# Kernel tuning notes

Measured on AMD Instinct MI355X. Metric: run time of the kernel, lower is better.

The kernel has to match this reference:

```python
import jax, jax.numpy as jnp
import numpy as np

N1, N2, D = 8192, 8192, 128

def setup_inputs() -> dict:
    key = jax.random.key(0)
    k1, k2 = jax.random.split(key)
    p1 = jax.random.normal(k1, (N1, D), dtype=jnp.float32)
    p2 = jax.random.normal(k2, (N2, D), dtype=jnp.float32)
    return {"p1": p1, "p2": p2}

def reference(p1, p2):
    # scores: [N1, N2]
    scores = jnp.matmul(p1, p2.T)
    # NOTE: original torch code MULTIPLIES by sqrt(N2) (not divide) — faithful.
    scale = jnp.asarray(scores.shape[-1], scores.dtype) ** 0.5
    weight = jax.nn.softmax(scores * scale, axis=-1)
    return jnp.matmul(weight, p2)  # [N1, D]
```

## Files before the change

kernel.cpp:

```cpp
#include <hip/hip_runtime.h>

#define NROWS 8192
#define DH 128
#define NTILES 256
#define NWAVES 4
#define BQ_WG 128
#define TILE_SHORTS 12288

typedef float f32x16 __attribute__((ext_vector_type(16)));
typedef float f32x4  __attribute__((ext_vector_type(4)));
typedef short s16x8  __attribute__((ext_vector_type(8)));

#define MFMA(a, b, c) __builtin_amdgcn_mfma_f32_32x32x16_bf16(a, b, c, 0, 0, 0)
#define EXP2F(x) __builtin_amdgcn_exp2f(x)

__device__ __forceinline__ short f2bf(float x) {
    unsigned u = __float_as_uint(x);
    unsigned r = (u + 0x7fffu + ((u >> 16) & 1u)) >> 16;
    return (short)r;
}
__device__ __forceinline__ float bf2f(short s) {
    return __uint_as_float(((unsigned)(unsigned short)s) << 16);
}

#define CSC 130.577849f

__device__ __forceinline__ void gload16(const short* g, short* l) {
    __builtin_amdgcn_global_load_lds(
        (const __attribute__((address_space(1))) unsigned*)g,
        (__attribute__((address_space(3))) unsigned*)l, 16, 0, 0);
}

__global__ __launch_bounds__(256) void prep(const float* __restrict__ KV,
                                            short* __restrict__ kws)
{
    const int t = blockIdx.x;
    const int tid = threadIdx.x;
    short* kh = kws + (size_t)t * TILE_SHORTS;
    short* kl = kh + 4096;
    short* vt = kh + 8192;

    {
        const int r  = tid >> 3;
        const int d0 = (tid & 7) << 4;
        const float* src = KV + ((size_t)(t * 32 + r)) * DH + d0;
        f32x4 a0 = *(const f32x4*)(src);
        f32x4 a1 = *(const f32x4*)(src + 4);
        f32x4 a2 = *(const f32x4*)(src + 8);
        f32x4 a3 = *(const f32x4*)(src + 12);
        s16x8 h0, h1, l0, l1;
        #pragma unroll
        for (int j = 0; j < 4; ++j) {
            { float x = a0[j]; short h = f2bf(x); h0[j]     = h; l0[j]     = f2bf(x - bf2f(h)); }
            { float x = a1[j]; short h = f2bf(x); h0[j + 4] = h; l0[j + 4] = f2bf(x - bf2f(h)); }
            { float x = a2[j]; short h = f2bf(x); h1[j]     = h; l1[j]     = f2bf(x - bf2f(h)); }
            { float x = a3[j]; short h = f2bf(x); h1[j + 4] = h; l1[j + 4] = f2bf(x - bf2f(h)); }
        }
        const int base = r * 128 + d0;
        const int swz  = (r & 7) << 3;
        *(s16x8*)&kh[(base    ) ^ swz] = h0;
        *(s16x8*)&kh[(base + 8) ^ swz] = h1;
        *(s16x8*)&kl[(base    ) ^ swz] = l0;
        *(s16x8*)&kl[(base + 8) ^ swz] = l1;
    }

    {
        const int pr = tid & 15;
        const int c8 = tid >> 4;
        const int r0 = pr * 2;
        const float* sa = KV + ((size_t)(t * 32 + r0)) * DH + c8 * 8;
        const float* sb = sa + DH;
        f32x4 a0 = *(const f32x4*)(sa);
        f32x4 a1 = *(const f32x4*)(sa + 4);
        f32x4 b0 = *(const f32x4*)(sb);
        f32x4 b1 = *(const f32x4*)(sb + 4);
        #pragma unroll
        for (int i = 0; i < 8; ++i) {
            int d = c8 * 8 + i;
            float xa = (i < 4) ? a0[i] : a1[i - 4];
            float xb = (i < 4) ? b0[i] : b1[i - 4];
            unsigned w = ((unsigned)(unsigned short)f2bf(xb) << 16) |
                         (unsigned short)f2bf(xa);
            int idx = (d * 32 + r0) ^ (((d >> 1) & 3) << 3);
            *(unsigned*)&vt[idx] = w;
        }
    }
}

__global__ __launch_bounds__(256, 2) void fa_partial(
    const float* __restrict__ Qm, const short* __restrict__ kws,
    float* __restrict__ Opart, float* __restrict__ mlbuf, int tiles_per_split)
{
    __shared__ __align__(16) short buf[2][TILE_SHORTS];
    __shared__ __align__(16) short pb[NWAVES][32 * 64];

    const int tid  = threadIdx.x;
    const int wid  = tid >> 6;
    const int lane = tid & 63;
    const int q32  = lane & 31;
    const int g    = lane >> 5;
    const int qb   = blockIdx.x;
    const int sp   = blockIdx.y;
    const int tile0 = sp * tiles_per_split;

    s16x8 qh[8], ql[8];
    {
        const float* qrow = Qm + ((size_t)(qb * BQ_WG + wid * 32 + q32)) * DH + g * 8;
        #pragma unroll
        for (int c = 0; c < 8; ++c) {
            const float* p = qrow + c * 16;
            f32x4 v0 = *(const f32x4*)(p);
            f32x4 v1 = *(const f32x4*)(p + 4);
            #pragma unroll
            for (int j = 0; j < 8; ++j) {
                float x = ((j < 4) ? v0[j] : v1[j - 4]) * CSC;
                short h = f2bf(x);
                qh[c][j] = h;
                ql[c][j] = f2bf(x - bf2f(h));
            }
        }
    }

    f32x16 oacc[4];
    #pragma unroll
    for (int b = 0; b < 4; ++b)
        #pragma unroll
        for (int i = 0; i < 16; ++i) oacc[b][i] = 0.0f;
    float mrun = -INFINITY;
    float lrun = 0.0f;

#define STAGE(bb, tt) do {                                              \
        const short* gs_ = kws + (size_t)(tt) * TILE_SHORTS + tid * 8;  \
        short* ld_ = &buf[bb][tid * 8];                                 \
        _Pragma("unroll")                                               \
        for (int ch_ = 0; ch_ < 6; ++ch_)                               \
            gload16(gs_ + ch_ * 2048, ld_ + ch_ * 2048);                \
    } while (0)

    int cur = 0;
    STAGE(0, tile0);

    for (int t = 0; t < tiles_per_split; ++t) {
        __syncthreads();
        if (t + 1 < tiles_per_split) STAGE(cur ^ 1, tile0 + t + 1);

        const short* kh = &buf[cur][0];
        const short* kl = &buf[cur][4096];
        const short* vt = &buf[cur][8192];

        f32x16 s;
        #pragma unroll
        for (int i = 0; i < 16; ++i) s[i] = 0.0f;
        #pragma unroll
        for (int c = 0; c < 8; ++c) {
            const int ia = (q32 * 128 + c * 16 + g * 8) ^ ((q32 & 7) << 3);
            s16x8 ah = *(const s16x8*)&kh[ia];
            s16x8 al = *(const s16x8*)&kl[ia];
            s = MFMA(ah, ql[c], s);
            s = MFMA(al, qh[c], s);
            s = MFMA(ah, qh[c], s);
        }

        float tmax = s[0];
        #pragma unroll
        for (int i = 1; i < 16; ++i) tmax = fmaxf(tmax, s[i]);
        tmax = fmaxf(tmax, __shfl_xor(tmax, 32));
        const float mnew  = fmaxf(mrun, tmax);
        const float alpha = EXP2F(mrun - mnew);
        float psum = 0.0f;
        #pragma unroll
        for (int i = 0; i < 16; ++i) { s[i] = EXP2F(s[i] - mnew); psum += s[i]; }
        psum += __shfl_xor(psum, 32);
        lrun = lrun * alpha + psum;
        if (__any(mnew > mrun)) {
            #pragma unroll
            for (int rI = 0; rI < 16; ++rI) {
                int qr = (rI & 3) + 8 * (rI >> 2) + 4 * g;
                float ar = __shfl(alpha, qr);
                #pragma unroll
                for (int b = 0; b < 4; ++b) oacc[b][rI] *= ar;
            }
        }
        mrun = mnew;

        {
            short* pw = pb[wid];
            #pragma unroll
            for (int pr2 = 0; pr2 < 8; ++pr2) {
                int rI = pr2 * 2;
                int k  = (rI & 3) + 8 * (rI >> 2) + 4 * g;
                unsigned w = ((unsigned)(unsigned short)f2bf(s[rI + 1]) << 16) |
                             (unsigned short)f2bf(s[rI]);
                int idx = (q32 * 64 + k) ^ ((q32 & 7) << 3);
                *(unsigned*)&pw[idx] = w;
            }
        }

        #pragma unroll
        for (int c2 = 0; c2 < 2; ++c2) {
            const int ip = (q32 * 64 + c2 * 16 + g * 8) ^ ((q32 & 7) << 3);
            s16x8 pa = *(const s16x8*)&pb[wid][ip];
            #pragma unroll
            for (int b = 0; b < 4; ++b) {
                int d  = b * 32 + q32;
                int iv = (d * 32 + c2 * 16 + g * 8) ^ (((d >> 1) & 3) << 3);
                s16x8 vv = *(const s16x8*)&vt[iv];
                oacc[b] = MFMA(pa, vv, oacc[b]);
            }
        }
        cur ^= 1;
    }
#undef STAGE

    {
        float* op = Opart + ((size_t)sp * NROWS + qb * BQ_WG + wid * 32) * DH;
        #pragma unroll
        for (int b = 0; b < 4; ++b)
            #pragma unroll
            for (int rI = 0; rI < 16; ++rI) {
                int qr = (rI & 3) + 8 * (rI >> 2) + 4 * g;
                op[qr * DH + b * 32 + q32] = oacc[b][rI];
            }
        if (lane < 32) {
            float2* mlp = (float2*)mlbuf;
            mlp[(size_t)sp * NROWS + qb * BQ_WG + wid * 32 + q32] = make_float2(mrun, lrun);
        }
    }
}

template <int NS>
__global__ __launch_bounds__(256) void fa_merge(const float* __restrict__ Opart,
                                               const float* __restrict__ mlbuf,
                                               float* __restrict__ out)
{
    int idx = blockIdx.x * 256 + threadIdx.x;
    int q   = idx >> 7;
    const float2* mlp = (const float2*)mlbuf;
    float2 mls[NS];
    float M = -INFINITY;
    #pragma unroll
    for (int s2 = 0; s2 < NS; ++s2) {
        mls[s2] = mlp[(size_t)s2 * NROWS + q];
        M = fmaxf(M, mls[s2].x);
    }
    float L = 0.0f, acc = 0.0f;
    #pragma unroll
    for (int s2 = 0; s2 < NS; ++s2) {
        float w = EXP2F(mls[s2].x - M);
        L   += w * mls[s2].y;
        acc += w * Opart[(size_t)s2 * NROWS * DH + idx];
    }
    out[idx] = acc / L;
}

extern "C" void kernel_launch(void* const* d_in, const int* in_sizes, int n_in,
                              void* d_out, int out_size, void* d_ws, size_t ws_size,
                              hipStream_t stream)
{
    const float* p1 = (const float*)d_in[0];
    const float* p2 = (const float*)d_in[1];
    float* out = (float*)d_out;

    const size_t kws_bytes  = (size_t)NTILES * TILE_SHORTS * sizeof(short);
    const size_t per_split  = (size_t)NROWS * DH * sizeof(float)
                            + (size_t)NROWS * 2 * sizeof(float);

    int nsplit = 1;
    const int cand[3] = {8, 4, 2};
    for (int i = 0; i < 3; ++i)
        if (kws_bytes + (size_t)cand[i] * per_split <= ws_size) { nsplit = cand[i]; break; }

    short* kws = (short*)d_ws;
    float* Opart;
    float* mlbuf;
    if (nsplit == 1) {
        Opart = out;
        mlbuf = (float*)((char*)d_ws + kws_bytes);
    } else {
        Opart = (float*)((char*)d_ws + kws_bytes);
        mlbuf = Opart + (size_t)nsplit * NROWS * DH;
    }

    prep<<<NTILES, 256, 0, stream>>>(p2, kws);

    dim3 grid1(NROWS / BQ_WG, nsplit);
    fa_partial<<<grid1, 256, 0, stream>>>(p1, kws, Opart, mlbuf, NTILES / nsplit);

    const int mgrid = (NROWS * DH) / 256;
    if (nsplit == 8)      fa_merge<8><<<mgrid, 256, 0, stream>>>(Opart, mlbuf, out);
    else if (nsplit == 4) fa_merge<4><<<mgrid, 256, 0, stream>>>(Opart, mlbuf, out);
    else if (nsplit == 2) fa_merge<2><<<mgrid, 256, 0, stream>>>(Opart, mlbuf, out);
    else                  fa_merge<1><<<mgrid, 256, 0, stream>>>(Opart, mlbuf, out);
}
```

Before: 156.3 us.

## Keep P in registers via permlane swap, lazy rescale, raise occupancy

Drops the per-wave LDS staging buffer for the softmax probabilities. P is converted with packed bf16 conversion and rearranged across half-waves with permlane32 swaps straight into the MFMA operand layout. Rescaling of the output accumulator is skipped unless the running max grows by more than a threshold, and launch bounds rise from 2 to 3 blocks per CU. A templated final path folds normalization in when there is no split. This removes LDS traffic and a sync point per tile, but raises register pressure and uses inline asm that must match the MFMA layout exactly.

After: 172.9 us. 1.11x slower.

```diff
diff --git a/kernel.cpp b/kernel.cpp
--- a/kernel.cpp
+++ b/kernel.cpp
@@ -24,6 +24,7 @@
 }
 
 #define CSC 130.577849f
+#define RESC_THR 8.0f
 
 __device__ __forceinline__ void gload16(const short* g, short* l) {
     __builtin_amdgcn_global_load_lds(
@@ -87,12 +88,12 @@
     }
 }
 
-__global__ __launch_bounds__(256, 2) void fa_partial(
+template <bool FINAL>
+__global__ __launch_bounds__(256, 3) void fa_partial(
     const float* __restrict__ Qm, const short* __restrict__ kws,
     float* __restrict__ Opart, float* __restrict__ mlbuf, int tiles_per_split)
 {
     __shared__ __align__(16) short buf[2][TILE_SHORTS];
-    __shared__ __align__(16) short pb[NWAVES][32 * 64];
 
     const int tid  = threadIdx.x;
     const int wid  = tid >> 6;
@@ -165,14 +166,12 @@
         #pragma unroll
         for (int i = 1; i < 16; ++i) tmax = fmaxf(tmax, s[i]);
         tmax = fmaxf(tmax, __shfl_xor(tmax, 32));
-        const float mnew  = fmaxf(mrun, tmax);
-        const float alpha = EXP2F(mrun - mnew);
-        float psum = 0.0f;
-        #pragma unroll
-        for (int i = 0; i < 16; ++i) { s[i] = EXP2F(s[i] - mnew); psum += s[i]; }
-        psum += __shfl_xor(psum, 32);
-        lrun = lrun * alpha + psum;
-        if (__any(mnew > mrun)) {
+
+        const bool resc = !__all(tmax <= mrun + RESC_THR);
+        float mnew = mrun, alpha = 1.0f;
+        if (resc) {
+            mnew  = fmaxf(mrun, tmax);
+            alpha = EXP2F(mrun - mnew);
             #pragma unroll
             for (int rI = 0; rI < 16; ++rI) {
                 int qr = (rI & 3) + 8 * (rI >> 2) + 4 * g;
@@ -181,38 +180,55 @@
                 for (int b = 0; b < 4; ++b) oacc[b][rI] *= ar;
             }
         }
+        float psum = 0.0f;
+        #pragma unroll
+        for (int i = 0; i < 16; ++i) { s[i] = EXP2F(s[i] - mnew); psum += s[i]; }
+        psum += __shfl_xor(psum, 32);
+        lrun = lrun * alpha + psum;
         mrun = mnew;
 
-        {
-            short* pw = pb[wid];
+        unsigned w[8];
+        #pragma unroll
+        for (int m = 0; m < 8; ++m)
+            asm("v_cvt_pk_bf16_f32 %0, %1, %2"
+                : "=v"(w[m]) : "v"(s[2 * m]), "v"(s[2 * m + 1]));
+        unsigned a0 = w[0], b0 = w[2];
+        asm("v_permlane32_swap_b32 %0, %1" : "+v"(a0), "+v"(b0));
+        unsigned c0 = w[1], d0 = w[3];
+        asm("v_permlane32_swap_b32 %0, %1" : "+v"(c0), "+v"(d0));
+        unsigned e0 = w[4], f0 = w[6];
+        asm("v_permlane32_swap_b32 %0, %1" : "+v"(e0), "+v"(f0));
+        unsigned g0 = w[5], h0 = w[7];
+        asm("v_permlane32_swap_b32 %0, %1" : "+v"(g0), "+v"(h0));
+        union { s16x8 v; unsigned u[4]; } pa0, pa1;
+        pa0.u[0] = a0; pa0.u[1] = c0; pa0.u[2] = b0; pa0.u[3] = d0;
+        pa1.u[0] = e0; pa1.u[1] = g0; pa1.u[2] = f0; pa1.u[3] = h0;
+
+        #pragma unroll
+        for (int b = 0; b < 4; ++b) {
+            const int d   = b * 32 + q32;
+            const int swv = ((d >> 1) & 3) << 3;
+            const int iv0 = (d * 32 + g * 8) ^ swv;
+            const int iv1 = (d * 32 + 16 + g * 8) ^ swv;
+            oacc[b] = MFMA(pa0.v, *(const s16x8*)&vt[iv0], oacc[b]);
+            oacc[b] = MFMA(pa1.v, *(const s16x8*)&vt[iv1], oacc[b]);
+        }
+        cur ^= 1;
+    }
+#undef STAGE
+
+    if (FINAL) {
+        const float inv = 1.0f / lrun;
+        float* op = Opart + ((size_t)(qb * BQ_WG + wid * 32)) * DH;
+        #pragma unroll
+        for (int b = 0; b < 4; ++b)
             #pragma unroll
-            for (int pr2 = 0; pr2 < 8; ++pr2) {
-                int rI = pr2 * 2;
-                int k  = (rI & 3) + 8 * (rI >> 2) + 4 * g;
-                unsigned w = ((unsigned)(unsigned short)f2bf(s[rI + 1]) << 16) |
-                             (unsigned short)f2bf(s[rI]);
-                int idx = (q32 * 64 + k) ^ ((q32 & 7) << 3);
-                *(unsigned*)&pw[idx] = w;
+            for (int rI = 0; rI < 16; ++rI) {
+                int qr = (rI & 3) + 8 * (rI >> 2) + 4 * g;
+                float ir = __shfl(inv, qr);
+                op[qr * DH + b * 32 + q32] = oacc[b][rI] * ir;
             }
-        }
-
-        #pragma unroll
-        for (int c2 = 0; c2 < 2; ++c2) {
-            const int ip = (q32 * 64 + c2 * 16 + g * 8) ^ ((q32 & 7) << 3);
-            s16x8 pa = *(const s16x8*)&pb[wid][ip];
-            #pragma unroll
-            for (int b = 0; b < 4; ++b) {
-                int d  = b * 32 + q32;
-                int iv = (d * 32 + c2 * 16 + g * 8) ^ (((d >> 1) & 3) << 3);
-                s16x8 vv = *(const s16x8*)&vt[iv];
-                oacc[b] = MFMA(pa, vv, oacc[b]);
-            }
-        }
-        cur ^= 1;
-    }
-#undef STAGE
-
-    {
+    } else {
         float* op = Opart + ((size_t)sp * NROWS + qb * BQ_WG + wid * 32) * DH;
         #pragma unroll
         for (int b = 0; b < 4; ++b)
@@ -271,24 +287,22 @@
         if (kws_bytes + (size_t)cand[i] * per_split <= ws_size) { nsplit = cand[i]; break; }
 
     short* kws = (short*)d_ws;
-    float* Opart;
-    float* mlbuf;
+    prep<<<NTILES, 256, 0, stream>>>(p2, kws);
+
     if (nsplit == 1) {
-        Opart = out;
-        mlbuf = (float*)((char*)d_ws + kws_bytes);
-    } else {
-        Opart = (float*)((char*)d_ws + kws_bytes);
-        mlbuf = Opart + (size_t)nsplit * NROWS * DH;
-    }
-
-    prep<<<NTILES, 256, 0, stream>>>(p2, kws);
+        dim3 grid1(NROWS / BQ_WG, 1);
+        fa_partial<true><<<grid1, 256, 0, stream>>>(p1, kws, out, nullptr, NTILES);
+        return;
+    }
+
+    float* Opart = (float*)((char*)d_ws + kws_bytes);
+    float* mlbuf = Opart + (size_t)nsplit * NROWS * DH;
 
     dim3 grid1(NROWS / BQ_WG, nsplit);
-    fa_partial<<<grid1, 256, 0, stream>>>(p1, kws, Opart, mlbuf, NTILES / nsplit);
+    fa_partial<false><<<grid1, 256, 0, stream>>>(p1, kws, Opart, mlbuf, NTILES / nsplit);
 
     const int mgrid = (NROWS * DH) / 256;
     if (nsplit == 8)      fa_merge<8><<<mgrid, 256, 0, stream>>>(Opart, mlbuf, out);
     else if (nsplit == 4) fa_merge<4><<<mgrid, 256, 0, stream>>>(Opart, mlbuf, out);
-    else if (nsplit == 2) fa_merge<2><<<mgrid, 256, 0, stream>>>(Opart, mlbuf, out);
-    else                  fa_merge<1><<<mgrid, 256, 0, stream>>>(Opart, mlbuf, out);
-}
+    else                  fa_merge<2><<<mgrid, 256, 0, stream>>>(Opart, mlbuf, out);
+}
```
